# Optimization experiments

Hardware: AMD Instinct MI355X
Metric: run time of the kernel (lower is better)

The kernel has to match this reference:

```python
import jax, jax.numpy as jnp
import numpy as np

BETA = 0.25


def setup_inputs() -> dict:
    key = jax.random.key(0)
    k1, k2 = jax.random.split(key)
    x = jax.random.normal(k1, (8, 256, 2048), dtype=jnp.float32)        # (B, C, L)
    codebook = jax.random.normal(k2, (8192, 256), dtype=jnp.float32)    # (K, C)
    return {"x": x, "codebook": codebook}


def reference(x, codebook):
    # x: (B, C, L) -> xt: (B, L, C)
    xt = jnp.transpose(x, (0, 2, 1))
    # Euclidean distances via ||a||^2 + ||b||^2 - 2 a.b (matches torch.cdist p=2)
    x_sq = jnp.sum(xt * xt, axis=-1, keepdims=True)          # (B, L, 1)
    c_sq = jnp.sum(codebook * codebook, axis=-1)             # (K,)
    dots = jnp.einsum('blc,kc->blk', xt, codebook)           # (B, L, K)
    dists = jnp.sqrt(jnp.maximum(x_sq + c_sq[None, None, :] - 2.0 * dots, 0.0))
    # NOTE: original code uses argmax over distances (faithfully reproduced)
    code = jnp.argmax(dists, axis=2)                         # (B, L) int
    emb = jnp.transpose(codebook[code], (0, 2, 1))           # (B, C, L)
    sg = jax.lax.stop_gradient
    loss = jnp.mean((sg(x) - emb) ** 2 + BETA * (sg(emb) - emb) ** 2)
    return code, emb, loss
```

## Files before the change

### kernel.cpp

```cpp
#include <hip/hip_runtime.h>
#include <hip/hip_fp16.h>
#include <stdint.h>

typedef unsigned int u32;
typedef unsigned long long u64;
typedef unsigned short ushort_t;

#define B_ 8
#define C_ 256
#define L_ 2048
#define K_ 8192
#define M_ 16384

#define WS_KEYS   0
#define WS_CNT    131072
#define WS_MAXCS  131076
#define WS_LOSS   131080
#define WS_XSQ    131328
#define WS_CSQ    196864
#define WS_LIST   295168
#define WS_LMAX   4489472
#define WS_XTH    12878080
#define WS_CBH    21266688
#define LIST_CAP  1048576u

typedef __attribute__((ext_vector_type(8))) short s8v;
typedef __attribute__((ext_vector_type(4))) float f4v;

__device__ __forceinline__ ushort_t f2bf(float f) {
  u32 u = __float_as_uint(f);
  u32 r = (u + 0x7FFFu + ((u >> 16) & 1u)) >> 16;
  return (ushort_t)r;
}

__device__ __forceinline__ void gld16(void* lds, const void* g) {
  __builtin_amdgcn_global_load_lds(
      (const __attribute__((address_space(1))) u32*)g,
      (__attribute__((address_space(3))) u32*)lds, 16, 0, 0);
}


__global__ void __launch_bounds__(256)
vq_transpose(const float* __restrict__ x, float* __restrict__ xtf,
             ushort_t* __restrict__ xth) {
  __shared__ float t[64][65];
  int tid = threadIdx.x;
  int b  = blockIdx.x >> 7;
  int cc = (blockIdx.x >> 5) & 3;
  int lc = blockIdx.x & 31;
#pragma unroll
  for (int j = 0; j < 4; ++j) {
    int c  = (tid >> 4) + j * 16;
    int lq = tid & 15;
    float4 v = *(const float4*)&x[((size_t)(b * C_ + cc * 64 + c)) * L_ + lc * 64 + lq * 4];
    t[c][lq * 4 + 0] = v.x; t[c][lq * 4 + 1] = v.y;
    t[c][lq * 4 + 2] = v.z; t[c][lq * 4 + 3] = v.w;
  }
  __syncthreads();
  int l = tid >> 2, qc = tid & 3;
  size_t m = (size_t)b * L_ + lc * 64 + l;
#pragma unroll
  for (int j = 0; j < 4; ++j) {
    int q = qc + j * 4;
    float4 v = make_float4(t[q * 4 + 0][l], t[q * 4 + 1][l],
                           t[q * 4 + 2][l], t[q * 4 + 3][l]);
    *(float4*)&xtf[m * C_ + cc * 64 + q * 4] = v;
    ushort4 h;
    h.x = f2bf(v.x); h.y = f2bf(v.y); h.z = f2bf(v.z); h.w = f2bf(v.w);
    *(ushort4*)&xth[m * C_ + cc * 64 + q * 4] = h;
  }
}

__global__ void vq_xsqt(const float* __restrict__ xtf, float* __restrict__ xsq) {
  int t = threadIdx.x;
  int m = blockIdx.x * 16 + (t >> 4);
  int g = t & 15;
  const float* row = xtf + (size_t)m * C_;
  float s = 0.0f;
#pragma unroll
  for (int j = 0; j < 4; ++j) {
    float4 v = *(const float4*)&row[g * 4 + j * 64];
    s += v.x * v.x + v.y * v.y + v.z * v.z + v.w * v.w;
  }
#pragma unroll
  for (int off = 1; off < 16; off <<= 1) s += __shfl_xor(s, off, 64);
  if (g == 0) xsq[m] = s;
}

__global__ void vq_cbprep(const float* __restrict__ cb, float* __restrict__ csq,
                          int* __restrict__ maxcs, ushort_t* __restrict__ cbh) {
  int t = threadIdx.x;
  int k = blockIdx.x * 16 + (t >> 4);
  int g = t & 15;
  const float* row = cb + (size_t)k * C_;
  float s = 0.0f;
#pragma unroll
  for (int j = 0; j < 4; ++j) {
    float4 v = *(const float4*)&row[g * 4 + j * 64];
    s += v.x * v.x + v.y * v.y + v.z * v.z + v.w * v.w;
    ushort4 h;
    h.x = f2bf(v.x); h.y = f2bf(v.y); h.z = f2bf(v.z); h.w = f2bf(v.w);
    *(ushort4*)&cbh[(size_t)k * C_ + g * 4 + j * 64] = h;
  }
#pragma unroll
  for (int off = 1; off < 16; off <<= 1) s += __shfl_xor(s, off, 64);
  if (g == 0) {
    csq[k] = s;
    atomicMax(maxcs, __float_as_int(s));
  }
}


#define STAGE(buf, t_)                                                        \
  {                                                                           \
    _Pragma("unroll")                                                         \
    for (int q = 0; q < 8; ++q) {                                             \
      int codeT = (w * 8 + q) * 2 + (l >> 5);                                 \
      int chunk = l & 31;                                                     \
      gld16(&Bs[(buf)][(w * 8 + q) * 512],                                    \
            &cbh[(size_t)(n0 + (t_) * 128 + codeT) * 256 +                    \
                 ((chunk ^ (codeT & 7)) * 8)]);                               \
    }                                                                         \
  }

__global__ void __launch_bounds__(512, 2)
vq_gemm(const ushort_t* __restrict__ xth, const ushort_t* __restrict__ cbh,
        const float* __restrict__ csq, __half* __restrict__ lmax) {
  __shared__ short Bs[2][128 * 256];

  const int tid = threadIdx.x;
  const int w = tid >> 6, l = tid & 63;
  const int lr = l & 15, lk = l >> 4;
  const int wr = w >> 1, wc = w & 1;
  const int strip = blockIdx.x >> 2, ns = blockIdx.x & 3;
  const int r0 = strip * 256 + wr * 64;
  const int n0 = ns * 2048;

  s8v a[4][8];
#pragma unroll
  for (int i = 0; i < 4; ++i)
#pragma unroll
    for (int ks = 0; ks < 8; ++ks)
      a[i][ks] = *(const s8v*)&xth[(size_t)(r0 + i * 16 + lr) * 256 + ks * 32 + lk * 8];

  STAGE(0, 0);
  __syncthreads();

  for (int t = 0; t < 16; ++t) {
    const int buf = t & 1;
    if (t < 15) STAGE(buf ^ 1, t + 1);

    f4v acc[4][4];
#pragma unroll
    for (int i = 0; i < 4; ++i)
#pragma unroll
      for (int j = 0; j < 4; ++j) acc[i][j] = (f4v){0.f, 0.f, 0.f, 0.f};

#pragma unroll
    for (int ks = 0; ks < 8; ++ks) {
      s8v b[4];
#pragma unroll
      for (int j = 0; j < 4; ++j) {
        int row = wc * 64 + j * 16 + lr;
        b[j] = *(const s8v*)&Bs[buf][row * 256 + (((ks * 4 + lk) ^ (lr & 7)) * 8)];
      }
#pragma unroll
      for (int i = 0; i < 4; ++i)
#pragma unroll
        for (int j = 0; j < 4; ++j)
          acc[i][j] = __builtin_amdgcn_mfma_f32_16x16x32_bf16(b[j], a[i][ks], acc[i][j], 0, 0, 0);
    }

    const int cbase = n0 + t * 128 + wc * 64;
    float vm[4][2];
#pragma unroll
    for (int jp = 0; jp < 2; ++jp) {
      float4 cqa = *(const float4*)&csq[cbase + jp * 32 + lk * 4];
      float4 cqb = *(const float4*)&csq[cbase + jp * 32 + 16 + lk * 4];
#pragma unroll
      for (int i = 0; i < 4; ++i) {
        f4v A0 = acc[i][2 * jp], A1 = acc[i][2 * jp + 1];
        float m0 = fmaxf(fmaxf(__fmaf_rn(-2.0f, A0[0], cqa.x),
                               __fmaf_rn(-2.0f, A0[1], cqa.y)),
                         fmaxf(__fmaf_rn(-2.0f, A0[2], cqa.z),
                               __fmaf_rn(-2.0f, A0[3], cqa.w)));
        float m1 = fmaxf(fmaxf(__fmaf_rn(-2.0f, A1[0], cqb.x),
                               __fmaf_rn(-2.0f, A1[1], cqb.y)),
                         fmaxf(__fmaf_rn(-2.0f, A1[2], cqb.z),
                               __fmaf_rn(-2.0f, A1[3], cqb.w)));
        float vmx = fmaxf(m0, m1);
        vmx = fmaxf(vmx, __shfl_xor(vmx, 16, 64));
        vmx = fmaxf(vmx, __shfl_xor(vmx, 32, 64));
        vm[i][jp] = vmx;
      }
    }
    if (l < 16) {
#pragma unroll
      for (int i = 0; i < 4; ++i) {
        short2 sv;
        sv.x = (short)__half_as_ushort(__float2half(vm[i][0]));
        sv.y = (short)__half_as_ushort(__float2half(vm[i][1]));
        *(short2*)&lmax[(size_t)(r0 + i * 16 + l) * 256 + ns * 64 + t * 4 + wc * 2] = sv;
      }
    }
    __syncthreads();
  }
}

__global__ void __launch_bounds__(256)
vq_thr(const __half* __restrict__ lmax, const float* __restrict__ xsq,
       const int* __restrict__ maxcs, u32* __restrict__ list, u32* __restrict__ cnt) {
  __shared__ u32 wcnt[4];
  __shared__ u32 gbase_s;
  const int t = threadIdx.x, w = t >> 6, l = t & 63;
  const int m0 = blockIdx.x * 64 + w * 16;
  const float mc = __int_as_float(*maxcs);

  ushort4 hv[16];
  float thv[16];
  u32 wtot = 0;
#pragma unroll
  for (int i = 0; i < 16; ++i) {
    int m = m0 + i;
    hv[i] = *(const ushort4*)&lmax[(size_t)m * 256 + l * 4];
    float v0 = __half2float(__ushort_as_half(hv[i].x));
    float v1 = __half2float(__ushort_as_half(hv[i].y));
    float v2 = __half2float(__ushort_as_half(hv[i].z));
    float v3 = __half2float(__ushort_as_half(hv[i].w));
    float g = fmaxf(fmaxf(v0, v1), fmaxf(v2, v3));
#pragma unroll
    for (int off = 1; off < 64; off <<= 1) g = fmaxf(g, __shfl_xor(g, off, 64));
    float th = g - (0.033f * sqrtf(xsq[m] * mc) + 0.6f);
    thv[i] = th;
    wtot += __popcll(__ballot(v0 >= th));
    wtot += __popcll(__ballot(v1 >= th));
    wtot += __popcll(__ballot(v2 >= th));
    wtot += __popcll(__ballot(v3 >= th));
  }
  if (l == 0) wcnt[w] = wtot;
  __syncthreads();
  if (t == 0) gbase_s = atomicAdd(cnt, wcnt[0] + wcnt[1] + wcnt[2] + wcnt[3]);
  __syncthreads();
  u32 off = gbase_s;
  for (int ww = 0; ww < w; ++ww) off += wcnt[ww];
#pragma unroll
  for (int i = 0; i < 16; ++i) {
    int m = m0 + i;
    float th = thv[i];
    float v[4];
    v[0] = __half2float(__ushort_as_half(hv[i].x));
    v[1] = __half2float(__ushort_as_half(hv[i].y));
    v[2] = __half2float(__ushort_as_half(hv[i].z));
    v[3] = __half2float(__ushort_as_half(hv[i].w));
#pragma unroll
    for (int j = 0; j < 4; ++j) {
      u64 mask = __ballot(v[j] >= th);
      if (v[j] >= th) {
        u32 pos = off + (u32)__popcll(mask & ((1ull << l) - 1ull));
        if (pos < LIST_CAP) list[pos] = ((u32)m << 8) | (u32)(l * 4 + j);
      }
      off += (u32)__popcll(mask);
    }
  }
}

__global__ void __launch_bounds__(256)
vq_rescore(const u32* __restrict__ list, const u32* __restrict__ cnt,
           const float* __restrict__ xtf, const float* __restrict__ cb,
           const float* __restrict__ xsq, const float* __restrict__ csq,
           u64* __restrict__ keys) {
  u32 n = *cnt; if (n > LIST_CAP) n = LIST_CAP;
  const int l = threadIdx.x & 63;
  const int u = l & 7;
  const int g = l >> 3;
  int wid = (blockIdx.x * 256 + threadIdx.x) >> 6;
  int nw = (gridDim.x * 256) >> 6;
  for (u32 e = wid; e < n; e += nw) {
    u32 ent = list[e];
    int m = (int)(ent >> 8), blk = (int)(ent & 255u);
    float4 xv[8];
#pragma unroll
    for (int i = 0; i < 8; ++i)
      xv[i] = *(const float4*)&xtf[(size_t)m * C_ + (i * 8 + u) * 4];
    float xq = xsq[m];
    u64 bestkey = 0;
#pragma unroll
    for (int cc = 0; cc < 4; ++cc) {
      int k = blk * 32 + cc * 8 + g;
      const float* crow = &cb[(size_t)k * C_];
      float p = 0.0f;
#pragma unroll
      for (int i = 0; i < 8; ++i) {
        float4 cv = *(const float4*)&crow[(i * 8 + u) * 4];
        p += xv[i].x * cv.x + xv[i].y * cv.y + xv[i].z * cv.z + xv[i].w * cv.w;
      }
#pragma unroll
      for (int off = 1; off < 8; off <<= 1) p += __shfl_xor(p, off, 64);
      if (u == 0) {
        float d2 = __fsub_rn(__fadd_rn(xq, csq[k]), __fmul_rn(2.0f, p));
        float dist = sqrtf(fmaxf(d2, 0.0f));
        u64 key = ((u64)__float_as_uint(dist) << 32) |
                  (u64)(0xFFFFFFFFu - (u32)k);
        if (key > bestkey) bestkey = key;
      }
    }
#pragma unroll
    for (int off = 8; off < 64; off <<= 1) {
      u64 o = __shfl_xor(bestkey, off, 64);
      if (o > bestkey) bestkey = o;
    }
    if (l == 0) atomicMax(&keys[m], bestkey);
  }
}


__global__ void __launch_bounds__(256)
vq_gather(const u64* __restrict__ keys, const float* __restrict__ cb,
          const float* __restrict__ x, float* __restrict__ out_code,
          float* __restrict__ emb, float* __restrict__ loss_acc) {
  __shared__ float rows[32 * 260];
  __shared__ int codes_s[32];
  __shared__ float partial[4];
  int t = threadIdx.x;
  int b = blockIdx.x >> 6;
  int l0 = (blockIdx.x & 63) * 32;
  if (t < 32) {
    u64 key = keys[b * L_ + l0 + t];
    int code = (int)(0xFFFFFFFFu - (u32)(key & 0xFFFFFFFFull));
    codes_s[t] = code;
    out_code[b * L_ + l0 + t] = (float)code;
  }
  __syncthreads();
  {
    int r = t >> 3, c4 = t & 7;
    const float* src = cb + (size_t)codes_s[r] * C_;
#pragma unroll
    for (int j = 0; j < 8; ++j) {
      float4 v = *(const float4*)&src[(c4 + 8 * j) * 4];
      *(float4*)&rows[r * 260 + (c4 + 8 * j) * 4] = v;
    }
  }
  __syncthreads();
  float ls = 0.0f;
  int l = t & 31, cg = t >> 5;
#pragma unroll 4
  for (int cs = 0; cs < 32; ++cs) {
    int c = cg * 32 + cs;
    float v = rows[l * 260 + c];
    size_t gi = (size_t)(b * C_ + c) * L_ + l0 + l;
    emb[gi] = v;
    float d = x[gi] - v;
    ls = fmaf(d, d, ls);
  }
#pragma unroll
  for (int off = 1; off < 64; off <<= 1) ls += __shfl_xor(ls, off, 64);
  if ((t & 63) == 0) partial[t >> 6] = ls;
  __syncthreads();
  if (t == 0)
    atomicAdd(loss_acc, partial[0] + partial[1] + partial[2] + partial[3]);
}

__global__ void vq_loss(const float* __restrict__ loss_acc, float* __restrict__ out) {
  out[0] = loss_acc[0] / 4194304.0f;
}

extern "C" void kernel_launch(void* const* d_in, const int* in_sizes, int n_in,
                              void* d_out, int out_size, void* d_ws, size_t ws_size,
                              hipStream_t stream) {
  const float* x  = (const float*)d_in[0];
  const float* cb = (const float*)d_in[1];
  float* out = (float*)d_out;
  char* ws = (char*)d_ws;

  u64* keys      = (u64*)(ws + WS_KEYS);
  u32* cnt       = (u32*)(ws + WS_CNT);
  int* maxcs     = (int*)(ws + WS_MAXCS);
  float* loss_a  = (float*)(ws + WS_LOSS);
  float* xsq     = (float*)(ws + WS_XSQ);
  float* csq     = (float*)(ws + WS_CSQ);
  u32* list      = (u32*)(ws + WS_LIST);
  __half* lmax   = (__half*)(ws + WS_LMAX);
  ushort_t* xth  = (ushort_t*)(ws + WS_XTH);
  ushort_t* cbh  = (ushort_t*)(ws + WS_CBH);
  float* xtf     = out + M_;

  hipMemsetAsync(ws, 0, 131084, stream);

  vq_transpose<<<1024, 256, 0, stream>>>(x, xtf, xth);
  vq_cbprep<<<K_ / 16, 256, 0, stream>>>(cb, csq, maxcs, cbh);
  vq_xsqt<<<M_ / 16, 256, 0, stream>>>(xtf, xsq);
  vq_gemm<<<256, 512, 0, stream>>>(xth, cbh, csq, lmax);
  vq_thr<<<256, 256, 0, stream>>>(lmax, xsq, maxcs, list, cnt);
  vq_rescore<<<2048, 256, 0, stream>>>(list, cnt, xtf, cb, xsq, csq, keys);
  vq_gather<<<(B_ * L_) / 32, 256, 0, stream>>>(keys, cb, x, out, out + M_, loss_a);
  vq_loss<<<1, 1, 0, stream>>>(loss_a, out + M_ + (size_t)B_ * C_ * L_);
}
```

Measured before the change: 248.3 us.

## Read codebook directly from global in GEMM and transpose block-max buffer

```diff
diff --git a/kernel.cpp b/kernel.cpp
--- a/kernel.cpp
+++ b/kernel.cpp
@@ -33,12 +33,6 @@
   return (ushort_t)r;
 }
 
-__device__ __forceinline__ void gld16(void* lds, const void* g) {
-  __builtin_amdgcn_global_load_lds(
-      (const __attribute__((address_space(1))) u32*)g,
-      (__attribute__((address_space(3))) u32*)lds, 16, 0, 0);
-}
-
 
 __global__ void __launch_bounds__(256)
 vq_transpose(const float* __restrict__ x, float* __restrict__ xtf,
@@ -111,23 +105,9 @@
 }
 
 
-#define STAGE(buf, t_)                                                        \
-  {                                                                           \
-    _Pragma("unroll")                                                         \
-    for (int q = 0; q < 8; ++q) {                                             \
-      int codeT = (w * 8 + q) * 2 + (l >> 5);                                 \
-      int chunk = l & 31;                                                     \
-      gld16(&Bs[(buf)][(w * 8 + q) * 512],                                    \
-            &cbh[(size_t)(n0 + (t_) * 128 + codeT) * 256 +                    \
-                 ((chunk ^ (codeT & 7)) * 8)]);                               \
-    }                                                                         \
-  }
-
 __global__ void __launch_bounds__(512, 2)
 vq_gemm(const ushort_t* __restrict__ xth, const ushort_t* __restrict__ cbh,
-        const float* __restrict__ csq, __half* __restrict__ lmax) {
-  __shared__ short Bs[2][128 * 256];
-
+        const float* __restrict__ csq, __half* __restrict__ lmaxt) {
   const int tid = threadIdx.x;
   const int w = tid >> 6, l = tid & 63;
   const int lr = l & 15, lk = l >> 4;
@@ -143,12 +123,8 @@
     for (int ks = 0; ks < 8; ++ks)
       a[i][ks] = *(const s8v*)&xth[(size_t)(r0 + i * 16 + lr) * 256 + ks * 32 + lk * 8];
 
-  STAGE(0, 0);
-  __syncthreads();
-
   for (int t = 0; t < 16; ++t) {
-    const int buf = t & 1;
-    if (t < 15) STAGE(buf ^ 1, t + 1);
+    const ushort_t* bbase = &cbh[(size_t)(n0 + t * 128 + wc * 64) * 256];
 
     f4v acc[4][4];
 #pragma unroll
@@ -160,10 +136,8 @@
     for (int ks = 0; ks < 8; ++ks) {
       s8v b[4];
 #pragma unroll
-      for (int j = 0; j < 4; ++j) {
-        int row = wc * 64 + j * 16 + lr;
-        b[j] = *(const s8v*)&Bs[buf][row * 256 + (((ks * 4 + lk) ^ (lr & 7)) * 8)];
-      }
+      for (int j = 0; j < 4; ++j)
+        b[j] = *(const s8v*)&bbase[(size_t)(j * 16 + lr) * 256 + (ks * 4 + lk) * 8];
 #pragma unroll
       for (int i = 0; i < 4; ++i)
 #pragma unroll
@@ -195,72 +169,51 @@
       }
     }
     if (l < 16) {
-#pragma unroll
-      for (int i = 0; i < 4; ++i) {
-        short2 sv;
-        sv.x = (short)__half_as_ushort(__float2half(vm[i][0]));
-        sv.y = (short)__half_as_ushort(__float2half(vm[i][1]));
-        *(short2*)&lmax[(size_t)(r0 + i * 16 + l) * 256 + ns * 64 + t * 4 + wc * 2] = sv;
-      }
-    }
-    __syncthreads();
+      const int colb = ns * 64 + t * 4 + wc * 2;
+#pragma unroll
+      for (int i = 0; i < 4; ++i)
+#pragma unroll
+        for (int jp = 0; jp < 2; ++jp)
+          lmaxt[(size_t)(colb + jp) * M_ + r0 + i * 16 + l] =
+              __ushort_as_half((ushort_t)__half_as_ushort(__float2half(vm[i][jp])));
+    }
   }
 }
 
 __global__ void __launch_bounds__(256)
-vq_thr(const __half* __restrict__ lmax, const float* __restrict__ xsq,
+vq_thr(const __half* __restrict__ lmaxt, const float* __restrict__ xsq,
        const int* __restrict__ maxcs, u32* __restrict__ list, u32* __restrict__ cnt) {
   __shared__ u32 wcnt[4];
   __shared__ u32 gbase_s;
-  const int t = threadIdx.x, w = t >> 6, l = t & 63;
-  const int m0 = blockIdx.x * 64 + w * 16;
-  const float mc = __int_as_float(*maxcs);
-
-  ushort4 hv[16];
-  float thv[16];
+  const int t = threadIdx.x, w = t >> 6;
+  const int m = blockIdx.x * 256 + t;
+
+  float g = -1e30f;
+  for (int c = 0; c < 256; ++c)
+    g = fmaxf(g, __half2float(lmaxt[(size_t)c * M_ + m]));
+  float th = g - (0.033f * sqrtf(xsq[m] * __int_as_float(*maxcs)) + 0.6f);
+
   u32 wtot = 0;
-#pragma unroll
-  for (int i = 0; i < 16; ++i) {
-    int m = m0 + i;
-    hv[i] = *(const ushort4*)&lmax[(size_t)m * 256 + l * 4];
-    float v0 = __half2float(__ushort_as_half(hv[i].x));
-    float v1 = __half2float(__ushort_as_half(hv[i].y));
-    float v2 = __half2float(__ushort_as_half(hv[i].z));
-    float v3 = __half2float(__ushort_as_half(hv[i].w));
-    float g = fmaxf(fmaxf(v0, v1), fmaxf(v2, v3));
-#pragma unroll
-    for (int off = 1; off < 64; off <<= 1) g = fmaxf(g, __shfl_xor(g, off, 64));
-    float th = g - (0.033f * sqrtf(xsq[m] * mc) + 0.6f);
-    thv[i] = th;
-    wtot += __popcll(__ballot(v0 >= th));
-    wtot += __popcll(__ballot(v1 >= th));
-    wtot += __popcll(__ballot(v2 >= th));
-    wtot += __popcll(__ballot(v3 >= th));
-  }
-  if (l == 0) wcnt[w] = wtot;
+  for (int c = 0; c < 256; ++c) {
+    float v = __half2float(lmaxt[(size_t)c * M_ + m]);
+    wtot += (u32)__popcll(__ballot(v >= th));
+  }
+  if ((t & 63) == 0) wcnt[w] = wtot;
   __syncthreads();
   if (t == 0) gbase_s = atomicAdd(cnt, wcnt[0] + wcnt[1] + wcnt[2] + wcnt[3]);
   __syncthreads();
   u32 off = gbase_s;
   for (int ww = 0; ww < w; ++ww) off += wcnt[ww];
-#pragma unroll
-  for (int i = 0; i < 16; ++i) {
-    int m = m0 + i;
-    float th = thv[i];
-    float v[4];
-    v[0] = __half2float(__ushort_as_half(hv[i].x));
-    v[1] = __half2float(__ushort_as_half(hv[i].y));
-    v[2] = __half2float(__ushort_as_half(hv[i].z));
-    v[3] = __half2float(__ushort_as_half(hv[i].w));
-#pragma unroll
-    for (int j = 0; j < 4; ++j) {
-      u64 mask = __ballot(v[j] >= th);
-      if (v[j] >= th) {
-        u32 pos = off + (u32)__popcll(mask & ((1ull << l) - 1ull));
-        if (pos < LIST_CAP) list[pos] = ((u32)m << 8) | (u32)(l * 4 + j);
-      }
-      off += (u32)__popcll(mask);
-    }
+
+  const u64 lanemask_lt = (1ull << (t & 63)) - 1ull;
+  for (int c = 0; c < 256; ++c) {
+    float v = __half2float(lmaxt[(size_t)c * M_ + m]);
+    u64 mask = __ballot(v >= th);
+    if (v >= th) {
+      u32 pos = off + (u32)__popcll(mask & lanemask_lt);
+      if (pos < LIST_CAP) list[pos] = ((u32)m << 8) | (u32)c;
+    }
+    off += (u32)__popcll(mask);
   }
 }
 
@@ -379,7 +332,7 @@
   float* xsq     = (float*)(ws + WS_XSQ);
   float* csq     = (float*)(ws + WS_CSQ);
   u32* list      = (u32*)(ws + WS_LIST);
-  __half* lmax   = (__half*)(ws + WS_LMAX);
+  __half* lmaxt  = (__half*)(ws + WS_LMAX);
   ushort_t* xth  = (ushort_t*)(ws + WS_XTH);
   ushort_t* cbh  = (ushort_t*)(ws + WS_CBH);
   float* xtf     = out + M_;
@@ -389,8 +342,8 @@
   vq_transpose<<<1024, 256, 0, stream>>>(x, xtf, xth);
   vq_cbprep<<<K_ / 16, 256, 0, stream>>>(cb, csq, maxcs, cbh);
   vq_xsqt<<<M_ / 16, 256, 0, stream>>>(xtf, xsq);
-  vq_gemm<<<256, 512, 0, stream>>>(xth, cbh, csq, lmax);
-  vq_thr<<<256, 256, 0, stream>>>(lmax, xsq, maxcs, list, cnt);
+  vq_gemm<<<256, 512, 0, stream>>>(xth, cbh, csq, lmaxt);
+  vq_thr<<<M_ / 256, 256, 0, stream>>>(lmaxt, xsq, maxcs, list, cnt);
   vq_rescore<<<2048, 256, 0, stream>>>(list, cnt, xtf, cb, xsq, csq, keys);
   vq_gather<<<(B_ * L_) / 32, 256, 0, stream>>>(keys, cb, x, out, out + M_, loss_a);
   vq_loss<<<1, 1, 0, stream>>>(loss_a, out + M_ + (size_t)B_ * C_ * L_);
```

New measurement: 348.9 us. 40.5% more time.
